# Kernel tuning notes

Measured on AMD Instinct MI355X. Metric: run time of the kernel, lower is better.

The kernel has to match this reference:

```python
import jax, jax.numpy as jnp
import numpy as np

E = 320000          # num edges
G = 256             # num graphs
NNF = 128           # node features
NEF = 64            # edge features
NGF = 64            # global features
HID = 128           # hidden channels
TGT = 64            # num targets
IN_CH = 2 * NNF + NEF + NGF  # 384


def setup_inputs() -> dict:
    key = jax.random.key(0)
    ks = jax.random.split(key, 10)
    ek = jax.random.normal(ks[0], (E, NEF), dtype=jnp.float32)
    vrk = jax.random.normal(ks[1], (E, NNF), dtype=jnp.float32)
    vsk = jax.random.normal(ks[2], (E, NNF), dtype=jnp.float32)
    u = jax.random.normal(ks[3], (G, NGF), dtype=jnp.float32)
    batch = jnp.sort(jax.random.randint(ks[4], (E,), 0, G, dtype=jnp.int64))
    # MLP params (Linear stores weight [out, in]; we keep [in, out] for x @ W)
    s1 = 1.0 / np.sqrt(IN_CH)
    s2 = 1.0 / np.sqrt(HID)
    W1 = jax.random.uniform(ks[5], (IN_CH, HID), jnp.float32, -s1, s1)
    b1 = jax.random.uniform(ks[6], (HID,), jnp.float32, -s1, s1)
    W2 = jax.random.uniform(ks[7], (HID, TGT), jnp.float32, -s2, s2)
    b2 = jax.random.uniform(ks[8], (TGT,), jnp.float32, -s2, s2)
    return {"ek": ek, "vrk": vrk, "vsk": vsk, "u": u, "batch": batch,
            "W1": W1, "b1": b1, "W2": W2, "b2": b2}


def reference(ek, vrk, vsk, u, batch, W1, b1, W2, b2):
    # gather per-edge global features, concat, 2-layer MLP with ReLU
    x = jnp.concatenate([ek, vrk, vsk, u[batch]], axis=1)  # [E, IN_CH]
    h = jax.nn.relu(x @ W1 + b1)                           # [E, HID]
    return h @ W2 + b2                                     # [E, TGT]
```

## Files before the change

kernel.cpp:

```cpp
#include <hip/hip_runtime.h>
#include <hip/hip_bf16.h>
#include <stdint.h>


typedef __bf16 bf16;
typedef __attribute__((ext_vector_type(8))) __bf16 bf16x8;
typedef __attribute__((ext_vector_type(4))) __bf16 bf16x4;
typedef __attribute__((ext_vector_type(4))) float floatx4;

__device__ __forceinline__ void ldg2lds16(const void* g, void* l) {
  __builtin_amdgcn_global_load_lds((__attribute__((address_space(1))) void*)g,
                                   (__attribute__((address_space(3))) void*)l,
                                   16, 0, 0);
}

__device__ __forceinline__ bf16x4 cvt_b4(floatx4 v) {
  bf16x4 r; r.x = (bf16)v.x; r.y = (bf16)v.y; r.z = (bf16)v.z; r.w = (bf16)v.w; return r;
}

__global__ void transpose_pre(const float* __restrict__ w1, bf16* __restrict__ w1t,
                              const float* __restrict__ w2, bf16* __restrict__ w2t) {
  __shared__ float t[32][33];
  int b = blockIdx.x;
  const float* src; bf16* dst; int R, C, tr, tc;
  if (b < 48) { src = w1; dst = w1t; R = 384; C = 128; tr = b >> 2; tc = b & 3; }
  else        { int bb = b - 48; src = w2; dst = w2t; R = 128; C = 64; tr = bb >> 1; tc = bb & 1; }
  int tx = threadIdx.x & 31, ty = threadIdx.x >> 5;
  #pragma unroll
  for (int i = 0; i < 32; i += 8)
    t[ty + i][tx] = src[(tr * 32 + ty + i) * C + tc * 32 + tx];
  __syncthreads();
  #pragma unroll
  for (int i = 0; i < 32; i += 8)
    dst[(tc * 32 + ty + i) * R + tr * 32 + tx] = (bf16)t[tx][ty + i];
}

__global__ __launch_bounds__(256, 3) void edge_mlp(
    const float* __restrict__ ek, const float* __restrict__ vrk, const float* __restrict__ vsk,
    const float* __restrict__ u, const int* __restrict__ batch,
    const bf16* __restrict__ w1t, const float* __restrict__ b1,
    const bf16* __restrict__ w2t, const float* __restrict__ b2,
    float* __restrict__ out)
{
  __shared__ __align__(16) bf16 smem[24576];
  bf16* x_lds  = smem;
  bf16* w1_lds = smem + 8192;
  bf16* h_lds  = smem;
  bf16* w2_lds = smem + 16384;

  const int tid  = threadIdx.x;
  const int lane = tid & 63;
  const int wv   = tid >> 6;
  const int m    = lane & 15;
  const int q    = lane >> 4;
  const int e0   = blockIdx.x * 128;

  const int hid_half  = (wv & 1) * 64;
  const int edge_half = (wv >> 1) * 64;

  const int srow8 = lane >> 3;
  const int sc8   = (lane & 7) ^ srow8;

  {
    const int r16 = lane >> 4;
    const int c16 = lane & 15;
    #pragma unroll
    for (int i = 0; i < 4; ++i) {
      int j = wv * 4 + i;
      int row = j * 4 + r16;
      int clog = c16 ^ (row & 15);
      ldg2lds16(w2t + row * 128 + clog * 8, w2_lds + j * 512);
    }
  }

  floatx4 bias1[4], bias2[2];
  #pragma unroll
  for (int hf = 0; hf < 4; ++hf)
    bias1[hf] = *(const floatx4*)(b1 + hid_half + hf * 16 + q * 4);
  const int tgt_half = (wv & 1) * 32;
  #pragma unroll
  for (int tf = 0; tf < 2; ++tf)
    bias2[tf] = *(const floatx4*)(b2 + tgt_half + tf * 16 + q * 4);

  floatx4 acc[4][4] = {};

  #pragma unroll
  for (int kc = 0; kc < 6; ++kc) {
    #pragma unroll
    for (int i = 0; i < 4; ++i) {
      int r0  = wv * 32 + i * 8;
      int row = r0 + srow8;
      ldg2lds16(w1t + (long)row * 384 + kc * 64 + sc8 * 8, w1_lds + r0 * 64);
    }
    #pragma unroll
    for (int j = 0; j < 8; ++j) {
      int f = tid + 256 * j;
      int r = f >> 4, c = f & 15;
      const float* srcp;
      if (kc == 0)      srcp = ek  + (long)(e0 + r) * 64;
      else if (kc == 1) srcp = vrk + (long)(e0 + r) * 128;
      else if (kc == 2) srcp = vrk + (long)(e0 + r) * 128 + 64;
      else if (kc == 3) srcp = vsk + (long)(e0 + r) * 128;
      else if (kc == 4) srcp = vsk + (long)(e0 + r) * 128 + 64;
      else              srcp = u   + (long)batch[e0 + r] * 64;
      floatx4 v = *(const floatx4*)(srcp + c * 4);
      int phys = (c >> 1) ^ (r & 7);
      *(bf16x4*)(x_lds + r * 64 + phys * 8 + (c & 1) * 4) = cvt_b4(v);
    }
    __syncthreads();
    #pragma unroll
    for (int ks = 0; ks < 2; ++ks) {
      bf16x8 af[4], bff[4];
      #pragma unroll
      for (int hf = 0; hf < 4; ++hf) {
        int hid  = hid_half + hf * 16 + m;
        int phys = (ks * 4 + q) ^ (hid & 7);
        af[hf] = *(const bf16x8*)(w1_lds + hid * 64 + phys * 8);
      }
      #pragma unroll
      for (int ef = 0; ef < 4; ++ef) {
        int edge = edge_half + ef * 16 + m;
        int phys = (ks * 4 + q) ^ (edge & 7);
        bff[ef] = *(const bf16x8*)(x_lds + edge * 64 + phys * 8);
      }
      #pragma unroll
      for (int hf = 0; hf < 4; ++hf)
        #pragma unroll
        for (int ef = 0; ef < 4; ++ef)
          acc[hf][ef] = __builtin_amdgcn_mfma_f32_16x16x32_bf16(af[hf], bff[ef], acc[hf][ef], 0, 0, 0);
    }
    __syncthreads();
  }

  #pragma unroll
  for (int hf = 0; hf < 4; ++hf) {
    int hid0 = hid_half + hf * 16 + q * 4;
    #pragma unroll
    for (int ef = 0; ef < 4; ++ef) {
      int edge = edge_half + ef * 16 + m;
      floatx4 v = acc[hf][ef] + bias1[hf];
      v.x = v.x > 0.f ? v.x : 0.f;
      v.y = v.y > 0.f ? v.y : 0.f;
      v.z = v.z > 0.f ? v.z : 0.f;
      v.w = v.w > 0.f ? v.w : 0.f;
      int c    = hid0 >> 3;
      int phys = c ^ (edge & 15);
      *(bf16x4*)(h_lds + edge * 128 + phys * 8 + (hid0 & 7)) = cvt_b4(v);
    }
  }
  __syncthreads();

  floatx4 acc2[2][4] = {};
  #pragma unroll
  for (int ks = 0; ks < 4; ++ks) {
    bf16x8 a2[2], bh[4];
    #pragma unroll
    for (int tf = 0; tf < 2; ++tf) {
      int tg   = tgt_half + tf * 16 + m;
      int phys = (ks * 4 + q) ^ (tg & 15);
      a2[tf] = *(const bf16x8*)(w2_lds + tg * 128 + phys * 8);
    }
    #pragma unroll
    for (int ef = 0; ef < 4; ++ef) {
      int ed   = edge_half + ef * 16 + m;
      int phys = (ks * 4 + q) ^ (ed & 15);
      bh[ef] = *(const bf16x8*)(h_lds + ed * 128 + phys * 8);
    }
    #pragma unroll
    for (int tf = 0; tf < 2; ++tf)
      #pragma unroll
      for (int ef = 0; ef < 4; ++ef)
        acc2[tf][ef] = __builtin_amdgcn_mfma_f32_16x16x32_bf16(a2[tf], bh[ef], acc2[tf][ef], 0, 0, 0);
  }

  #pragma unroll
  for (int tf = 0; tf < 2; ++tf) {
    int tgt0 = tgt_half + tf * 16 + q * 4;
    #pragma unroll
    for (int ef = 0; ef < 4; ++ef) {
      int ed = edge_half + ef * 16 + m;
      floatx4 v = acc2[tf][ef] + bias2[tf];
      *(floatx4*)(out + (long)(e0 + ed) * 64 + tgt0) = v;
    }
  }
}

extern "C" void kernel_launch(void* const* d_in, const int* in_sizes, int n_in,
                              void* d_out, int out_size, void* d_ws, size_t ws_size,
                              hipStream_t stream) {
  const float* ek    = (const float*)d_in[0];
  const float* vrk   = (const float*)d_in[1];
  const float* vsk   = (const float*)d_in[2];
  const float* u     = (const float*)d_in[3];
  const int*   batch = (const int*)d_in[4];
  const float* W1    = (const float*)d_in[5];
  const float* b1    = (const float*)d_in[6];
  const float* W2    = (const float*)d_in[7];
  const float* b2    = (const float*)d_in[8];
  float* out = (float*)d_out;

  bf16* w1t = (bf16*)d_ws;
  bf16* w2t = (bf16*)d_ws + 128 * 384;

  transpose_pre<<<56, 256, 0, stream>>>(W1, w1t, W2, w2t);
  edge_mlp<<<2500, 256, 0, stream>>>(ek, vrk, vsk, u, batch, w1t, b1, w2t, b2, out);
}
```

Baseline: 460.7 us.

## Load MFMA operands directly from global with fragment-packed weights, per-wave tiles

Weights are pre-packed into MFMA-fragment order so each lane loads its A fragment straight from global/L2, and each wave independently handles 32 edges, loading its X fragments straight from global and converting to bf16 in registers. This removes the LDS staging of X and W1 and all block-wide barriers, and raises occupancy to 4 blocks. The hidden activations and the output go through per-wave LDS to stay coalesced. In exchange, the weight fragments are reread from global by every wave, and the X loads use a less coalesced 32-byte-per-lane pattern.

```diff
diff --git a/kernel.cpp b/kernel.cpp
--- a/kernel.cpp
+++ b/kernel.cpp
@@ -8,180 +8,153 @@
 typedef __attribute__((ext_vector_type(4))) __bf16 bf16x4;
 typedef __attribute__((ext_vector_type(4))) float floatx4;
 
-__device__ __forceinline__ void ldg2lds16(const void* g, void* l) {
-  __builtin_amdgcn_global_load_lds((__attribute__((address_space(1))) void*)g,
-                                   (__attribute__((address_space(3))) void*)l,
-                                   16, 0, 0);
+__device__ __forceinline__ bf16x8 cvt_b8(floatx4 a, floatx4 b) {
+  bf16x8 r;
+  r[0] = (bf16)a.x; r[1] = (bf16)a.y; r[2] = (bf16)a.z; r[3] = (bf16)a.w;
+  r[4] = (bf16)b.x; r[5] = (bf16)b.y; r[6] = (bf16)b.z; r[7] = (bf16)b.w;
+  return r;
+}
+__device__ __forceinline__ bf16x4 cvt_b4(floatx4 v) {
+  bf16x4 r;
+  r[0] = (bf16)v.x; r[1] = (bf16)v.y; r[2] = (bf16)v.z; r[3] = (bf16)v.w;
+  return r;
 }
 
-__device__ __forceinline__ bf16x4 cvt_b4(floatx4 v) {
-  bf16x4 r; r.x = (bf16)v.x; r.y = (bf16)v.y; r.z = (bf16)v.z; r.w = (bf16)v.w; return r;
+__global__ void pack_pre(const float* __restrict__ W1, bf16* __restrict__ w1p,
+                         const float* __restrict__ W2, bf16* __restrict__ w2p) {
+  int b = blockIdx.x, lane = threadIdx.x;
+  int mm = lane & 15, qq = lane >> 4;
+  if (b < 96) {
+    int kc = b >> 3, hf = b & 7;
+    bf16x8 r;
+    #pragma unroll
+    for (int j = 0; j < 8; ++j)
+      r[j] = (bf16)W1[(kc * 32 + qq * 8 + j) * 128 + hf * 16 + mm];
+    *(bf16x8*)(w1p + ((long)b * 64 + lane) * 8) = r;
+  } else {
+    int bb = b - 96;
+    int ks = bb >> 2, tf = bb & 3;
+    bf16x8 r;
+    #pragma unroll
+    for (int j = 0; j < 8; ++j)
+      r[j] = (bf16)W2[(ks * 32 + qq * 8 + j) * 64 + tf * 16 + mm];
+    *(bf16x8*)(w2p + ((long)bb * 64 + lane) * 8) = r;
+  }
 }
 
-__global__ void transpose_pre(const float* __restrict__ w1, bf16* __restrict__ w1t,
-                              const float* __restrict__ w2, bf16* __restrict__ w2t) {
-  __shared__ float t[32][33];
-  int b = blockIdx.x;
-  const float* src; bf16* dst; int R, C, tr, tc;
-  if (b < 48) { src = w1; dst = w1t; R = 384; C = 128; tr = b >> 2; tc = b & 3; }
-  else        { int bb = b - 48; src = w2; dst = w2t; R = 128; C = 64; tr = bb >> 1; tc = bb & 1; }
-  int tx = threadIdx.x & 31, ty = threadIdx.x >> 5;
-  #pragma unroll
-  for (int i = 0; i < 32; i += 8)
-    t[ty + i][tx] = src[(tr * 32 + ty + i) * C + tc * 32 + tx];
-  __syncthreads();
-  #pragma unroll
-  for (int i = 0; i < 32; i += 8)
-    dst[(tc * 32 + ty + i) * R + tr * 32 + tx] = (bf16)t[tx][ty + i];
-}
-
-__global__ __launch_bounds__(256, 3) void edge_mlp(
+__global__ __launch_bounds__(256, 4) void edge_mlp(
     const float* __restrict__ ek, const float* __restrict__ vrk, const float* __restrict__ vsk,
     const float* __restrict__ u, const int* __restrict__ batch,
-    const bf16* __restrict__ w1t, const float* __restrict__ b1,
-    const bf16* __restrict__ w2t, const float* __restrict__ b2,
+    const bf16* __restrict__ w1p, const float* __restrict__ b1,
+    const bf16* __restrict__ w2p, const float* __restrict__ b2,
     float* __restrict__ out)
 {
-  __shared__ __align__(16) bf16 smem[24576];
-  bf16* x_lds  = smem;
-  bf16* w1_lds = smem + 8192;
-  bf16* h_lds  = smem;
-  bf16* w2_lds = smem + 16384;
-
+  __shared__ __align__(16) bf16 smem[16384];
   const int tid  = threadIdx.x;
   const int lane = tid & 63;
   const int wv   = tid >> 6;
   const int m    = lane & 15;
   const int q    = lane >> 4;
-  const int e0   = blockIdx.x * 128;
+  bf16* hs = smem + wv * 4096;
 
-  const int hid_half  = (wv & 1) * 64;
-  const int edge_half = (wv >> 1) * 64;
+  const int e0 = blockIdx.x * 128 + wv * 32;
 
-  const int srow8 = lane >> 3;
-  const int sc8   = (lane & 7) ^ srow8;
+  const float* px[4][2];
+  #pragma unroll
+  for (int ef = 0; ef < 2; ++ef) {
+    int e = e0 + ef * 16 + m;
+    px[0][ef] = ek  + (long)e * 64  + q * 8;
+    px[1][ef] = vrk + (long)e * 128 + q * 8;
+    px[2][ef] = vsk + (long)e * 128 + q * 8;
+    px[3][ef] = u   + (long)batch[e] * 64 + q * 8;
+  }
+  const bf16* wp = w1p + lane * 8;
 
-  {
-    const int r16 = lane >> 4;
-    const int c16 = lane & 15;
+  floatx4 acc[8][2] = {};
+  #pragma unroll
+  for (int kc = 0; kc < 12; ++kc) {
+    const int src = (kc < 2) ? 0 : (kc < 6) ? 1 : (kc < 10) ? 2 : 3;
+    const int off = (kc < 2) ? kc * 32
+                  : (kc < 6) ? (kc - 2) * 32
+                  : (kc < 10) ? (kc - 6) * 32 : (kc - 10) * 32;
+    bf16x8 xb[2];
     #pragma unroll
-    for (int i = 0; i < 4; ++i) {
-      int j = wv * 4 + i;
-      int row = j * 4 + r16;
-      int clog = c16 ^ (row & 15);
-      ldg2lds16(w2t + row * 128 + clog * 8, w2_lds + j * 512);
+    for (int ef = 0; ef < 2; ++ef) {
+      floatx4 v0 = *(const floatx4*)(px[src][ef] + off);
+      floatx4 v1 = *(const floatx4*)(px[src][ef] + off + 4);
+      xb[ef] = cvt_b8(v0, v1);
+    }
+    #pragma unroll
+    for (int hf = 0; hf < 8; ++hf) {
+      bf16x8 af = *(const bf16x8*)(wp + (kc * 8 + hf) * 512);
+      acc[hf][0] = __builtin_amdgcn_mfma_f32_16x16x32_bf16(af, xb[0], acc[hf][0], 0, 0, 0);
+      acc[hf][1] = __builtin_amdgcn_mfma_f32_16x16x32_bf16(af, xb[1], acc[hf][1], 0, 0, 0);
     }
   }
 
-  floatx4 bias1[4], bias2[2];
   #pragma unroll
-  for (int hf = 0; hf < 4; ++hf)
-    bias1[hf] = *(const floatx4*)(b1 + hid_half + hf * 16 + q * 4);
-  const int tgt_half = (wv & 1) * 32;
-  #pragma unroll
-  for (int tf = 0; tf < 2; ++tf)
-    bias2[tf] = *(const floatx4*)(b2 + tgt_half + tf * 16 + q * 4);
-
-  floatx4 acc[4][4] = {};
-
-  #pragma unroll
-  for (int kc = 0; kc < 6; ++kc) {
+  for (int hf = 0; hf < 8; ++hf) {
+    floatx4 b1v = *(const floatx4*)(b1 + hf * 16 + q * 4);
     #pragma unroll
-    for (int i = 0; i < 4; ++i) {
-      int r0  = wv * 32 + i * 8;
-      int row = r0 + srow8;
-      ldg2lds16(w1t + (long)row * 384 + kc * 64 + sc8 * 8, w1_lds + r0 * 64);
-    }
-    #pragma unroll
-    for (int j = 0; j < 8; ++j) {
-      int f = tid + 256 * j;
-      int r = f >> 4, c = f & 15;
-      const float* srcp;
-      if (kc == 0)      srcp = ek  + (long)(e0 + r) * 64;
-      else if (kc == 1) srcp = vrk + (long)(e0 + r) * 128;
-      else if (kc == 2) srcp = vrk + (long)(e0 + r) * 128 + 64;
-      else if (kc == 3) srcp = vsk + (long)(e0 + r) * 128;
-      else if (kc == 4) srcp = vsk + (long)(e0 + r) * 128 + 64;
-      else              srcp = u   + (long)batch[e0 + r] * 64;
-      floatx4 v = *(const floatx4*)(srcp + c * 4);
-      int phys = (c >> 1) ^ (r & 7);
-      *(bf16x4*)(x_lds + r * 64 + phys * 8 + (c & 1) * 4) = cvt_b4(v);
-    }
-    __syncthreads();
-    #pragma unroll
-    for (int ks = 0; ks < 2; ++ks) {
-      bf16x8 af[4], bff[4];
-      #pragma unroll
-      for (int hf = 0; hf < 4; ++hf) {
-        int hid  = hid_half + hf * 16 + m;
-        int phys = (ks * 4 + q) ^ (hid & 7);
-        af[hf] = *(const bf16x8*)(w1_lds + hid * 64 + phys * 8);
-      }
-      #pragma unroll
-      for (int ef = 0; ef < 4; ++ef) {
-        int edge = edge_half + ef * 16 + m;
-        int phys = (ks * 4 + q) ^ (edge & 7);
-        bff[ef] = *(const bf16x8*)(x_lds + edge * 64 + phys * 8);
-      }
-      #pragma unroll
-      for (int hf = 0; hf < 4; ++hf)
-        #pragma unroll
-        for (int ef = 0; ef < 4; ++ef)
-          acc[hf][ef] = __builtin_amdgcn_mfma_f32_16x16x32_bf16(af[hf], bff[ef], acc[hf][ef], 0, 0, 0);
-    }
-    __syncthreads();
-  }
-
-  #pragma unroll
-  for (int hf = 0; hf < 4; ++hf) {
-    int hid0 = hid_half + hf * 16 + q * 4;
-    #pragma unroll
-    for (int ef = 0; ef < 4; ++ef) {
-      int edge = edge_half + ef * 16 + m;
-      floatx4 v = acc[hf][ef] + bias1[hf];
+    for (int ef = 0; ef < 2; ++ef) {
+      floatx4 v = acc[hf][ef] + b1v;
       v.x = v.x > 0.f ? v.x : 0.f;
       v.y = v.y > 0.f ? v.y : 0.f;
       v.z = v.z > 0.f ? v.z : 0.f;
       v.w = v.w > 0.f ? v.w : 0.f;
-      int c    = hid0 >> 3;
-      int phys = c ^ (edge & 15);
-      *(bf16x4*)(h_lds + edge * 128 + phys * 8 + (hid0 & 7)) = cvt_b4(v);
+      int r_e  = ef * 16 + m;
+      int c    = hf * 2 + (q >> 1);
+      int phys = c ^ (r_e & 15);
+      *(bf16x4*)(hs + r_e * 128 + phys * 8 + (q & 1) * 4) = cvt_b4(v);
     }
   }
-  __syncthreads();
+  asm volatile("s_waitcnt lgkmcnt(0)" ::: "memory");
+  __builtin_amdgcn_sched_barrier(0);
 
-  floatx4 acc2[2][4] = {};
+  floatx4 acc2[4][2] = {};
+  const bf16* wq = w2p + lane * 8;
   #pragma unroll
   for (int ks = 0; ks < 4; ++ks) {
-    bf16x8 a2[2], bh[4];
+    bf16x8 hb[2];
     #pragma unroll
-    for (int tf = 0; tf < 2; ++tf) {
-      int tg   = tgt_half + tf * 16 + m;
-      int phys = (ks * 4 + q) ^ (tg & 15);
-      a2[tf] = *(const bf16x8*)(w2_lds + tg * 128 + phys * 8);
+    for (int ef = 0; ef < 2; ++ef) {
+      int r_e  = ef * 16 + m;
+      int phys = (ks * 4 + q) ^ (r_e & 15);
+      hb[ef] = *(const bf16x8*)(hs + r_e * 128 + phys * 8);
     }
     #pragma unroll
-    for (int ef = 0; ef < 4; ++ef) {
-      int ed   = edge_half + ef * 16 + m;
-      int phys = (ks * 4 + q) ^ (ed & 15);
-      bh[ef] = *(const bf16x8*)(h_lds + ed * 128 + phys * 8);
+    for (int tf = 0; tf < 4; ++tf) {
+      bf16x8 a2 = *(const bf16x8*)(wq + (ks * 4 + tf) * 512);
+      acc2[tf][0] = __builtin_amdgcn_mfma_f32_16x16x32_bf16(a2, hb[0], acc2[tf][0], 0, 0, 0);
+      acc2[tf][1] = __builtin_amdgcn_mfma_f32_16x16x32_bf16(a2, hb[1], acc2[tf][1], 0, 0, 0);
     }
-    #pragma unroll
-    for (int tf = 0; tf < 2; ++tf)
-      #pragma unroll
-      for (int ef = 0; ef < 4; ++ef)
-        acc2[tf][ef] = __builtin_amdgcn_mfma_f32_16x16x32_bf16(a2[tf], bh[ef], acc2[tf][ef], 0, 0, 0);
   }
 
+  asm volatile("s_waitcnt lgkmcnt(0)" ::: "memory");
+  __builtin_amdgcn_sched_barrier(0);
+  float* fs = (float*)hs;
   #pragma unroll
-  for (int tf = 0; tf < 2; ++tf) {
-    int tgt0 = tgt_half + tf * 16 + q * 4;
+  for (int tf = 0; tf < 4; ++tf) {
+    floatx4 b2v = *(const floatx4*)(b2 + tf * 16 + q * 4);
     #pragma unroll
-    for (int ef = 0; ef < 4; ++ef) {
-      int ed = edge_half + ef * 16 + m;
-      floatx4 v = acc2[tf][ef] + bias2[tf];
-      *(floatx4*)(out + (long)(e0 + ed) * 64 + tgt0) = v;
+    for (int ef = 0; ef < 2; ++ef) {
+      floatx4 v = acc2[tf][ef] + b2v;
+      int r_e  = ef * 16 + m;
+      int c    = tf * 4 + q;
+      int phys = c ^ (r_e & 15);
+      *(floatx4*)(fs + r_e * 64 + phys * 4) = v;
     }
+  }
+  asm volatile("s_waitcnt lgkmcnt(0)" ::: "memory");
+  __builtin_amdgcn_sched_barrier(0);
+
+  float* outp = out + (long)e0 * 64;
+  #pragma unroll
+  for (int i = 0; i < 8; ++i) {
+    int r_e  = i * 4 + q;
+    int phys = m ^ (r_e & 15);
+    floatx4 v = *(const floatx4*)(fs + r_e * 64 + phys * 4);
+    *(floatx4*)(outp + i * 256 + lane * 4) = v;
   }
 }
 
@@ -199,9 +172,9 @@
   const float* b2    = (const float*)d_in[8];
   float* out = (float*)d_out;
 
-  bf16* w1t = (bf16*)d_ws;
-  bf16* w2t = (bf16*)d_ws + 128 * 384;
+  bf16* w1p = (bf16*)d_ws;
+  bf16* w2p = (bf16*)d_ws + 49152;
 
-  transpose_pre<<<56, 256, 0, stream>>>(W1, w1t, W2, w2t);
-  edge_mlp<<<2500, 256, 0, stream>>>(ek, vrk, vsk, u, batch, w1t, b1, w2t, b2, out);
+  pack_pre<<<112, 64, 0, stream>>>(W1, w1p, W2, w2p);
+  edge_mlp<<<2500, 256, 0, stream>>>(ek, vrk, vsk, u, batch, w1p, b1, w2p, b2, out);
 }
```

Result: no change. 469.7 us (+2.0%).
